# Performance work log

Hardware: AMD Instinct MI355X
Metric: run time of the kernel (lower is better)

Reference implementation:

```python
import jax, jax.numpy as jnp
import numpy as np

N, K, H = 20000, 32, 128
DIN = 3 * H   # num_hidden + num_in = 128 + 256
FF = 4 * H
SCALE = 30.0
EPS = 1e-5


def setup_inputs() -> dict:
    key = jax.random.key(0)
    ks = jax.random.split(key, 32)
    s = 0.05
    w = lambda k, shp: jax.random.normal(k, shp, dtype=jnp.float32) * s
    return {
        "h_V": jax.random.normal(ks[0], (N, H), dtype=jnp.float32),
        "h_E": jax.random.normal(ks[1], (N, K, H), dtype=jnp.float32),
        "mask_V": jnp.ones((N,), dtype=jnp.float32),
        "mask_attend": jnp.ones((N, K), dtype=jnp.float32),
        # message MLP 1 (weights stored [in, out])
        "W1_w": w(ks[2], (DIN, H)), "W1_b": jnp.zeros((H,)),
        "W2_w": w(ks[3], (H, H)),   "W2_b": jnp.zeros((H,)),
        "W3_w": w(ks[4], (H, H)),   "W3_b": jnp.zeros((H,)),
        # message MLP 2
        "W11_w": w(ks[5], (DIN, H)), "W11_b": jnp.zeros((H,)),
        "W12_w": w(ks[6], (H, H)),   "W12_b": jnp.zeros((H,)),
        "W13_w": w(ks[7], (H, H)),   "W13_b": jnp.zeros((H,)),
        # position-wise FFN
        "Win_w": w(ks[8], (H, FF)),  "Win_b": jnp.zeros((FF,)),
        "Wout_w": w(ks[9], (FF, H)), "Wout_b": jnp.zeros((H,)),
        # LayerNorms
        "ln1_g": jnp.ones((H,)), "ln1_b": jnp.zeros((H,)),
        "ln2_g": jnp.ones((H,)), "ln2_b": jnp.zeros((H,)),
        "ln3_g": jnp.ones((H,)), "ln3_b": jnp.zeros((H,)),
        "E_idx": jax.random.randint(ks[10], (N, K), 0, N),
    }


def _ln(x, g, b):
    m = jnp.mean(x, -1, keepdims=True)
    v = jnp.mean(jnp.square(x - m), -1, keepdims=True)
    return (x - m) * jax.lax.rsqrt(v + EPS) * g + b


def _gelu(x):
    return jax.nn.gelu(x, approximate=False)  # torch default (erf) GELU


def reference(h_V, h_E, mask_V, mask_attend,
              W1_w, W1_b, W2_w, W2_b, W3_w, W3_b,
              W11_w, W11_b, W12_w, W12_b, W13_w, W13_b,
              Win_w, Win_b, Wout_w, Wout_b,
              ln1_g, ln1_b, ln2_g, ln2_b, ln3_g, ln3_b,
              E_idx):
    n, k = E_idx.shape

    def edge_feats(hv):
        nbr = hv[E_idx]  # [N,K,H] gather of neighbor node features
        hv_exp = jnp.broadcast_to(hv[:, None, :], (n, k, hv.shape[-1]))
        return jnp.concatenate([hv_exp, h_E, nbr], -1)  # [N,K,3H]

    # --- node update ---
    h_EV = edge_feats(h_V)
    msg = _gelu(h_EV @ W1_w + W1_b)
    msg = _gelu(msg @ W2_w + W2_b)
    msg = msg @ W3_w + W3_b
    msg = mask_attend[..., None] * msg
    dh = jnp.sum(msg, axis=-2) / SCALE
    hV = _ln(h_V + dh, ln1_g, ln1_b)
    dh = _gelu(hV @ Win_w + Win_b) @ Wout_w + Wout_b
    hV = _ln(hV + dh, ln2_g, ln2_b)
    hV = mask_V[:, None] * hV

    # --- edge update ---
    h_EV = edge_feats(hV)
    msg = _gelu(h_EV @ W11_w + W11_b)
    msg = _gelu(msg @ W12_w + W12_b)
    msg = msg @ W13_w + W13_b
    hE = _ln(h_E + msg, ln3_g, ln3_b)
    return (hV, hE)
```

## Files before the change

### kernel.cpp

```cpp
#include <hip/hip_runtime.h>
#include <hip/hip_bf16.h>
#include <cstdint>
#include <cstddef>

#define NN 20000
#define KK 32
#define HH 128
#define FFD 512
#define LN_EPS 1e-5f

typedef __attribute__((ext_vector_type(8))) short bf16x8;
typedef __attribute__((ext_vector_type(4))) float f32x4;

__device__ __forceinline__ short f2b(float f){
  __hip_bfloat16 h = __float2bfloat16(f);
  return __builtin_bit_cast(short, h);
}
__device__ __forceinline__ float b2f(short s){
  union { unsigned int u; float f; } v; v.u = ((unsigned int)(unsigned short)s) << 16; return v.f;
}
__device__ __forceinline__ unsigned int pk2(float a, float b){
  return (unsigned int)(unsigned short)f2b(a) | ((unsigned int)(unsigned short)f2b(b) << 16);
}
__device__ __forceinline__ float gelu_fast(float x){
  float u = x * __builtin_fmaf(0.10294278f, x*x, 2.3022082f);
  float e = __builtin_amdgcn_exp2f(u);
  float r = __builtin_amdgcn_rcpf(1.0f + e);
  return __builtin_fmaf(-x, r, x);
}
__device__ __forceinline__ f32x4 MFMA(bf16x8 a, bf16x8 b, f32x4 c){
  return __builtin_amdgcn_mfma_f32_16x16x32_bf16(a, b, c, 0, 0, 0);
}

__global__ __launch_bounds__(256) void enc_pack(
    const float* __restrict__ W1, const float* __restrict__ W2, const float* __restrict__ W3,
    const float* __restrict__ W11, const float* __restrict__ W12, const float* __restrict__ W13,
    const float* __restrict__ Win, const float* __restrict__ Wout,
    short* __restrict__ pk)
{
  const int stride = gridDim.x * blockDim.x;
  for (int idx = blockIdx.x*blockDim.x + threadIdx.x; idx < 294912; idx += stride){
    const float* src = W2; int srow = 0, k, n, NT, NCOLS, base;
    if (idx < 163840){
      int slot = idx >> 14, e = idx & 16383;
      k = e >> 7; n = e & 127; NT = 8; NCOLS = 128; base = slot << 14;
      switch (slot){
        case 0: src = W1;  srow = 0;   break;
        case 1: src = W1;  srow = 256; break;
        case 2: src = W1;  srow = 128; break;
        case 3: src = W2;  srow = 0;   break;
        case 4: src = W3;  srow = 0;   break;
        case 5: src = W11; srow = 0;   break;
        case 6: src = W11; srow = 256; break;
        case 7: src = W11; srow = 128; break;
        case 8: src = W12; srow = 0;   break;
        default: src = W13; srow = 0;  break;
      }
    } else if (idx < 229376){
      int e = idx - 163840; k = e >> 9; n = e & 511; NT = 32; NCOLS = 512; src = Win; base = 163840;
    } else {
      int e = idx - 229376; k = e >> 7; n = e & 127; NT = 8; NCOLS = 128; src = Wout; base = 229376;
    }
    float v = src[(srow + k)*NCOLS + n];
    int out = base + (((k>>5)*NT + (n>>4))*64 + ((k>>3)&3)*16 + (n&15))*8 + (k&7);
    pk[out] = f2b(v);
  }
}

__global__ __launch_bounds__(256, 2) void enc_proj(
    const float* __restrict__ X, const short* __restrict__ pkU, const short* __restrict__ pkZ,
    const float* __restrict__ biasU, short* __restrict__ U, short* __restrict__ Z)
{
  const int lane = threadIdx.x & 63, w = threadIdx.x >> 6;
  const int kgrp = lane >> 4, ccol = lane & 15;
  const int row0 = blockIdx.x*64 + w*16;
  const int arow = row0 + (lane & 15);
  f32x4 accU[8], accZ[8];
  #pragma unroll
  for (int nf=0;nf<8;nf++){ accU[nf] = (f32x4){0,0,0,0}; accZ[nf] = (f32x4){0,0,0,0}; }
  #pragma unroll
  for (int kt=0;kt<4;kt++){
    bf16x8 af = {0,0,0,0,0,0,0,0};
    if (arow < NN){
      const float4* p = (const float4*)(X + (size_t)arow*HH + kt*32 + kgrp*8);
      float4 v0 = p[0], v1 = p[1];
      af[0]=f2b(v0.x); af[1]=f2b(v0.y); af[2]=f2b(v0.z); af[3]=f2b(v0.w);
      af[4]=f2b(v1.x); af[5]=f2b(v1.y); af[6]=f2b(v1.z); af[7]=f2b(v1.w);
    }
    #pragma unroll
    for (int nf=0;nf<8;nf++){
      bf16x8 bu = *(const bf16x8*)(pkU + (((kt<<3)+nf)*64 + lane)*8);
      accU[nf] = MFMA(af, bu, accU[nf]);
      bf16x8 bz = *(const bf16x8*)(pkZ + (((kt<<3)+nf)*64 + lane)*8);
      accZ[nf] = MFMA(af, bz, accZ[nf]);
    }
  }
  #pragma unroll
  for (int nf=0;nf<8;nf++){
    #pragma unroll
    for (int r=0;r<4;r++){
      int grow = row0 + kgrp*4 + r;
      if (grow < NN){
        int col = nf*16 + ccol;
        U[(size_t)grow*HH + col] = f2b(accU[nf][r] + biasU[col]);
        Z[(size_t)grow*HH + col] = f2b(accZ[nf][r]);
      }
    }
  }
}

#define LSTR 136
template<int PASS>
__global__ __launch_bounds__(256, 3) void enc_mlp3(
    const float* __restrict__ hE,
    const short* __restrict__ Ub, const short* __restrict__ Zb,
    const int*  __restrict__ Eidx,
    const float* __restrict__ maskAtt,
    const float* __restrict__ hV,
    const float* __restrict__ lnG, const float* __restrict__ lnB,
    const short* __restrict__ pkL1,
    const short* __restrict__ pkL2, const float* __restrict__ bias2,
    const short* __restrict__ pkL3, const float* __restrict__ bias3,
    float* __restrict__ outP)
{
  __shared__ __align__(16) short sBuf[64*LSTR];
  __shared__ __align__(16) short sW[16384];
  __shared__ float sB23[256];
  __shared__ float sPart[4][128];

  const int i0 = blockIdx.x*2;
  const int t = threadIdx.x;
  const int lane = t & 63, w = t >> 6;
  const int kgrp = lane >> 4, ccol = lane & 15;
  const int g = w >> 1;
  const int rw = w*16;

  const int zrow = rw + (lane >> 2);
  const int seg0 = lane & 3;
  const int j = Eidx[i0*KK + zrow];
  const int4* zsrc = (const int4*)(Zb + (size_t)j*HH);

  float ureg[8];
  #pragma unroll
  for (int nf=0; nf<8; nf++) ureg[nf] = b2f(Ub[(size_t)(i0+g)*HH + nf*16 + ccol]);

  float mreg[4] = {0,0,0,0};
  if (PASS == 0){
    const float4 mv = *(const float4*)(maskAtt + i0*KK + rw + kgrp*4);
    mreg[0]=mv.x; mreg[1]=mv.y; mreg[2]=mv.z; mreg[3]=mv.w;
  }

  sB23[t] = (t < 128) ? bias2[t] : bias3[t-128];

  #pragma unroll
  for (int it=0; it<8; it++){
    int idx = it*256 + t;
    *(int4*)(sW + idx*8) = *(const int4*)(pkL1 + idx*8);
  }

  {
    const float4* src = (const float4*)(hE + ((size_t)i0*KK + rw)*HH);
    #pragma unroll
    for (int it=0; it<8; it++){
      int r = it*2 + (lane>>5);
      int c4 = lane & 31;
      float4 v = src[r*32 + c4];
      uint2 p; p.x = pk2(v.x, v.y); p.y = pk2(v.z, v.w);
      *(uint2*)(sBuf + (rw + r)*LSTR + c4*4) = p;
    }
  }
  __syncthreads();

  const short* sRow = sBuf + (rw + ccol)*LSTR;
  f32x4 acc[8];

  #pragma unroll
  for (int nf=0;nf<8;nf++) acc[nf] = (f32x4){ureg[nf],ureg[nf],ureg[nf],ureg[nf]};
  #pragma unroll
  for (int kt=0;kt<4;kt++){
    bf16x8 af = *(const bf16x8*)(sRow + kt*32 + kgrp*8);
    #pragma unroll
    for (int nf=0;nf<8;nf++){
      bf16x8 b = *(const bf16x8*)(sW + (((kt<<3)+nf)*64 + lane)*8);
      acc[nf] = MFMA(af, b, acc[nf]);
    }
  }
  {
    int4 z0 = zsrc[seg0];
    int4 z1 = zsrc[seg0 + 4];
    int4 z2 = zsrc[seg0 + 8];
    int4 z3 = zsrc[seg0 + 12];
    *(int4*)(sBuf + zrow*LSTR + (seg0     )*8) = z0;
    *(int4*)(sBuf + zrow*LSTR + (seg0 + 4 )*8) = z1;
    *(int4*)(sBuf + zrow*LSTR + (seg0 + 8 )*8) = z2;
    *(int4*)(sBuf + zrow*LSTR + (seg0 + 12)*8) = z3;
  }
  __syncthreads();
  #pragma unroll
  for (int it=0; it<8; it++){
    int idx = it*256 + t;
    *(int4*)(sW + idx*8) = *(const int4*)(pkL2 + idx*8);
  }
  #pragma unroll
  for (int nf=0;nf<8;nf++){
    #pragma unroll
    for (int r=0;r<4;r++){
      short* p = sBuf + (rw + kgrp*4 + r)*LSTR + nf*16 + ccol;
      float v = acc[nf][r] + b2f(*p);
      *p = f2b(gelu_fast(v));
    }
  }
  __syncthreads();

  #pragma unroll
  for (int nf=0;nf<8;nf++){
    float b2v = sB23[nf*16 + ccol];
    acc[nf] = (f32x4){b2v,b2v,b2v,b2v};
  }
  #pragma unroll
  for (int kt=0;kt<4;kt++){
    bf16x8 af = *(const bf16x8*)(sRow + kt*32 + kgrp*8);
    #pragma unroll
    for (int nf=0;nf<8;nf++){
      bf16x8 b = *(const bf16x8*)(sW + (((kt<<3)+nf)*64 + lane)*8);
      acc[nf] = MFMA(af, b, acc[nf]);
    }
  }
  __syncthreads();
  #pragma unroll
  for (int it=0; it<8; it++){
    int idx = it*256 + t;
    *(int4*)(sW + idx*8) = *(const int4*)(pkL3 + idx*8);
  }
  #pragma unroll
  for (int nf=0;nf<8;nf++){
    #pragma unroll
    for (int r=0;r<4;r++){
      short* p = sBuf + (rw + kgrp*4 + r)*LSTR + nf*16 + ccol;
      *p = f2b(gelu_fast(acc[nf][r]));
    }
  }
  __syncthreads();

  #pragma unroll
  for (int nf=0;nf<8;nf++){
    float b3v = sB23[128 + nf*16 + ccol];
    acc[nf] = (f32x4){b3v,b3v,b3v,b3v};
  }
  #pragma unroll
  for (int kt=0;kt<4;kt++){
    bf16x8 af = *(const bf16x8*)(sRow + kt*32 + kgrp*8);
    #pragma unroll
    for (int nf=0;nf<8;nf++){
      bf16x8 b = *(const bf16x8*)(sW + (((kt<<3)+nf)*64 + lane)*8);
      acc[nf] = MFMA(af, b, acc[nf]);
    }
  }

  if (PASS == 0){
    float ps[8];
    #pragma unroll
    for (int nf=0;nf<8;nf++){
      float s = 0.f;
      #pragma unroll
      for (int r=0;r<4;r++) s = __builtin_fmaf(acc[nf][r], mreg[r], s);
      s += __shfl_xor(s, 16);
      s += __shfl_xor(s, 32);
      ps[nf] = s;
    }
    if (kgrp == 0){
      #pragma unroll
      for (int nf=0;nf<8;nf++) sPart[w][nf*16 + ccol] = ps[nf];
    }
    __syncthreads();
    if ((w & 1) == 0){
      const int node = i0 + (w>>1);
      float c0 = sPart[w][lane]    + sPart[w+1][lane];
      float c1 = sPart[w][64+lane] + sPart[w+1][64+lane];
      float x0 = hV[(size_t)node*HH + lane]      + c0*(1.0f/30.0f);
      float x1 = hV[(size_t)node*HH + 64 + lane] + c1*(1.0f/30.0f);
      float sm = x0 + x1, sq = x0*x0 + x1*x1;
      #pragma unroll
      for (int off=1; off<64; off<<=1){
        sm += __shfl_xor(sm, off);
        sq += __shfl_xor(sq, off);
      }
      float mean = sm*(1.f/128.f);
      float var  = sq*(1.f/128.f) - mean*mean;
      float inv  = rsqrtf(var + LN_EPS);
      outP[(size_t)node*HH + lane]      = (x0-mean)*inv*lnG[lane]    + lnB[lane];
      outP[(size_t)node*HH + 64 + lane] = (x1-mean)*inv*lnG[64+lane] + lnB[64+lane];
    }
  } else {
    float rs[4] = {0,0,0,0}, rq[4] = {0,0,0,0};
    #pragma unroll
    for (int nf=0;nf<8;nf++){
      #pragma unroll
      for (int r=0;r<4;r++){
        int row = rw + kgrp*4 + r, col = nf*16 + ccol;
        float x = acc[nf][r] + hE[((size_t)(i0*KK + row))*HH + col];
        acc[nf][r] = x;
        rs[r] += x; rq[r] += x*x;
      }
    }
    #pragma unroll
    for (int off=1; off<16; off<<=1){
      #pragma unroll
      for (int r=0;r<4;r++){
        rs[r] += __shfl_xor(rs[r], off);
        rq[r] += __shfl_xor(rq[r], off);
      }
    }
    #pragma unroll
    for (int r=0;r<4;r++){
      float mean = rs[r]*(1.f/128.f);
      float var  = rq[r]*(1.f/128.f) - mean*mean;
      float inv  = rsqrtf(var + LN_EPS);
      #pragma unroll
      for (int nf=0;nf<8;nf++){
        int row = rw + kgrp*4 + r, col = nf*16 + ccol;
        outP[((size_t)(i0*KK + row))*HH + col] = (acc[nf][r]-mean)*inv*lnG[col] + lnB[col];
      }
    }
  }
}

__global__ __launch_bounds__(256, 2) void enc_ffn(
    const float* __restrict__ X,
    const short* __restrict__ pkWin, const float* __restrict__ bin,
    const short* __restrict__ pkWout, const float* __restrict__ bout,
    const float* __restrict__ g2, const float* __restrict__ b2ln,
    const float* __restrict__ maskV,
    float* __restrict__ out)
{
  __shared__ short sT[64*512];
  const int t = threadIdx.x, lane = t & 63, w = t >> 6;
  const int kgrp = lane >> 4, ccol = lane & 15;
  const int row0 = blockIdx.x*64;
  const int arow = row0 + w*16 + (lane & 15);
  f32x4 acc[32];
  #pragma unroll
  for (int nf=0;nf<32;nf++) acc[nf] = (f32x4){0,0,0,0};
  #pragma unroll
  for (int kt=0;kt<4;kt++){
    bf16x8 af = {0,0,0,0,0,0,0,0};
    if (arow < NN){
      const float4* p = (const float4*)(X + (size_t)arow*HH + kt*32 + kgrp*8);
      float4 v0 = p[0], v1 = p[1];
      af[0]=f2b(v0.x); af[1]=f2b(v0.y); af[2]=f2b(v0.z); af[3]=f2b(v0.w);
      af[4]=f2b(v1.x); af[5]=f2b(v1.y); af[6]=f2b(v1.z); af[7]=f2b(v1.w);
    }
    #pragma unroll
    for (int nf=0;nf<32;nf++){
      bf16x8 b = *(const bf16x8*)(pkWin + ((size_t)((kt<<5)+nf)*64 + lane)*8);
      acc[nf] = MFMA(af, b, acc[nf]);
    }
  }
  #pragma unroll
  for (int nf=0;nf<32;nf++){
    #pragma unroll
    for (int r=0;r<4;r++){
      int rl = w*16 + kgrp*4 + r, col = nf*16 + ccol;
      sT[rl*512 + (col ^ ((rl&7)<<3))] = f2b(gelu_fast(acc[nf][r] + bin[col]));
    }
  }
  f32x4 a2[8];
  #pragma unroll
  for (int nf=0;nf<8;nf++) a2[nf] = (f32x4){0,0,0,0};
  const int rl_a = w*16 + (lane & 15);
  #pragma unroll
  for (int kt=0;kt<16;kt++){
    int base = kt*32 + kgrp*8;
    bf16x8 af = *(const bf16x8*)(sT + rl_a*512 + (base ^ ((rl_a&7)<<3)));
    #pragma unroll
    for (int nf=0;nf<8;nf++){
      bf16x8 b = *(const bf16x8*)(pkWout + (((kt<<3)+nf)*64 + lane)*8);
      a2[nf] = MFMA(af, b, a2[nf]);
    }
  }
  float rsum[4] = {0,0,0,0}, rsq[4] = {0,0,0,0};
  #pragma unroll
  for (int nf=0;nf<8;nf++){
    #pragma unroll
    for (int r=0;r<4;r++){
      int grow = row0 + w*16 + kgrp*4 + r, col = nf*16 + ccol;
      float prev = (grow < NN) ? X[(size_t)grow*HH + col] : 0.f;
      float x = a2[nf][r] + bout[col] + prev;
      a2[nf][r] = x;
      rsum[r] += x; rsq[r] += x*x;
    }
  }
  #pragma unroll
  for (int off=1; off<16; off<<=1){
    #pragma unroll
    for (int r=0;r<4;r++){
      rsum[r] += __shfl_xor(rsum[r], off);
      rsq[r]  += __shfl_xor(rsq[r], off);
    }
  }
  #pragma unroll
  for (int r=0;r<4;r++){
    int grow = row0 + w*16 + kgrp*4 + r;
    float mean = rsum[r]*(1.f/128.f);
    float var  = rsq[r]*(1.f/128.f) - mean*mean;
    float inv  = rsqrtf(var + LN_EPS);
    float mv   = (grow < NN) ? maskV[grow] : 0.f;
    #pragma unroll
    for (int nf=0;nf<8;nf++){
      int col = nf*16 + ccol;
      if (grow < NN)
        out[(size_t)grow*HH + col] = mv * ((a2[nf][r]-mean)*inv*g2[col] + b2ln[col]);
    }
  }
}

extern "C" void kernel_launch(void* const* d_in, const int* in_sizes, int n_in,
                              void* d_out, int out_size, void* d_ws, size_t ws_size,
                              hipStream_t stream)
{
  const float* h_V   = (const float*)d_in[0];
  const float* h_E   = (const float*)d_in[1];
  const float* maskV = (const float*)d_in[2];
  const float* maskA = (const float*)d_in[3];
  const float* W1w  = (const float*)d_in[4];  const float* W1b  = (const float*)d_in[5];
  const float* W2w  = (const float*)d_in[6];  const float* W2b  = (const float*)d_in[7];
  const float* W3w  = (const float*)d_in[8];  const float* W3b  = (const float*)d_in[9];
  const float* W11w = (const float*)d_in[10]; const float* W11b = (const float*)d_in[11];
  const float* W12w = (const float*)d_in[12]; const float* W12b = (const float*)d_in[13];
  const float* W13w = (const float*)d_in[14]; const float* W13b = (const float*)d_in[15];
  const float* Winw = (const float*)d_in[16]; const float* Winb = (const float*)d_in[17];
  const float* Woutw= (const float*)d_in[18]; const float* Woutb= (const float*)d_in[19];
  const float* ln1g = (const float*)d_in[20]; const float* ln1b = (const float*)d_in[21];
  const float* ln2g = (const float*)d_in[22]; const float* ln2b = (const float*)d_in[23];
  const float* ln3g = (const float*)d_in[24]; const float* ln3b = (const float*)d_in[25];
  const int*   Eidx = (const int*)d_in[26];

  float* outV = (float*)d_out;
  float* outE = outV + (size_t)NN*HH;

  char* ws = (char*)d_ws;
  short* pk = (short*)ws;
  const short* pkW1a  = pk + 0*16384;
  const short* pkW1c  = pk + 1*16384;
  const short* pkW1bb = pk + 2*16384;
  const short* pkW2   = pk + 3*16384;
  const short* pkW3   = pk + 4*16384;
  const short* pkW11a = pk + 5*16384;
  const short* pkW11c = pk + 6*16384;
  const short* pkW11bb= pk + 7*16384;
  const short* pkW12  = pk + 8*16384;
  const short* pkW13  = pk + 9*16384;
  const short* pkWin  = pk + 163840;
  const short* pkWout = pk + 229376;

  short* U1 = (short*)(ws + 1048576);
  short* Z1 = (short*)(ws + 6291456);
  short* U2 = (short*)(ws + 11534336);
  short* Z2 = (short*)(ws + 16777216);
  float* hVmid = (float*)(ws + 22020096);

  enc_pack<<<288, 256, 0, stream>>>(W1w, W2w, W3w, W11w, W12w, W13w, Winw, Woutw, pk);
  enc_proj<<<313, 256, 0, stream>>>(h_V, pkW1a, pkW1c, W1b, U1, Z1);
  enc_mlp3<0><<<NN/2, 256, 0, stream>>>(h_E, U1, Z1, Eidx, maskA, h_V,
                                        ln1g, ln1b, pkW1bb, pkW2, W2b, pkW3, W3b, hVmid);
  enc_ffn<<<313, 256, 0, stream>>>(hVmid, pkWin, Winb, pkWout, Woutb,
                                   ln2g, ln2b, maskV, outV);
  enc_proj<<<313, 256, 0, stream>>>(outV, pkW11a, pkW11c, W11b, U2, Z2);
  enc_mlp3<1><<<NN/2, 256, 0, stream>>>(h_E, U2, Z2, Eidx, nullptr, nullptr,
                                        ln3g, ln3b, pkW11bb, pkW12, W12b, pkW13, W13b, outE);
}
```

Baseline: 439.3 us.

## Process four nodes per 512-thread block in edge MLP kernel

Doubles the block size of the fused edge MLP kernel so each block handles four nodes (128 edge rows) instead of two. Each staged weight matrix in shared memory is then reused across twice as many rows, halving weight-staging traffic per edge. Bias and U-term additions move from accumulator initialisation into the epilogues, and the Z/U/mask loads are deferred, to reduce live registers. Shared memory per block grows and the launch bound changes to 512 threads with 4 blocks requested, which may be infeasible and could hurt occupancy or cause spills.

Result: faster. 424.6 us (-3.3%).

```diff
diff --git a/kernel.cpp b/kernel.cpp
--- a/kernel.cpp
+++ b/kernel.cpp
@@ -111,7 +111,7 @@
 
 #define LSTR 136
 template<int PASS>
-__global__ __launch_bounds__(256, 3) void enc_mlp3(
+__global__ __launch_bounds__(512, 4) void enc_mlp3(
     const float* __restrict__ hE,
     const short* __restrict__ Ub, const short* __restrict__ Zb,
     const int*  __restrict__ Eidx,
@@ -123,38 +123,23 @@
     const short* __restrict__ pkL3, const float* __restrict__ bias3,
     float* __restrict__ outP)
 {
-  __shared__ __align__(16) short sBuf[64*LSTR];
+  __shared__ __align__(16) short sBuf[128*LSTR];
   __shared__ __align__(16) short sW[16384];
   __shared__ float sB23[256];
-  __shared__ float sPart[4][128];
-
-  const int i0 = blockIdx.x*2;
+  __shared__ float sPart[8][128];
+
+  const int i0 = blockIdx.x*4;
   const int t = threadIdx.x;
   const int lane = t & 63, w = t >> 6;
   const int kgrp = lane >> 4, ccol = lane & 15;
-  const int g = w >> 1;
+  const int node = i0 + (w >> 1);
   const int rw = w*16;
 
-  const int zrow = rw + (lane >> 2);
-  const int seg0 = lane & 3;
-  const int j = Eidx[i0*KK + zrow];
-  const int4* zsrc = (const int4*)(Zb + (size_t)j*HH);
-
-  float ureg[8];
-  #pragma unroll
-  for (int nf=0; nf<8; nf++) ureg[nf] = b2f(Ub[(size_t)(i0+g)*HH + nf*16 + ccol]);
-
-  float mreg[4] = {0,0,0,0};
-  if (PASS == 0){
-    const float4 mv = *(const float4*)(maskAtt + i0*KK + rw + kgrp*4);
-    mreg[0]=mv.x; mreg[1]=mv.y; mreg[2]=mv.z; mreg[3]=mv.w;
-  }
-
-  sB23[t] = (t < 128) ? bias2[t] : bias3[t-128];
-
-  #pragma unroll
-  for (int it=0; it<8; it++){
-    int idx = it*256 + t;
+  if (t < 256) sB23[t] = (t < 128) ? bias2[t] : bias3[t-128];
+
+  #pragma unroll
+  for (int it=0; it<4; it++){
+    int idx = it*512 + t;
     *(int4*)(sW + idx*8) = *(const int4*)(pkL1 + idx*8);
   }
 
@@ -175,7 +160,7 @@
   f32x4 acc[8];
 
   #pragma unroll
-  for (int nf=0;nf<8;nf++) acc[nf] = (f32x4){ureg[nf],ureg[nf],ureg[nf],ureg[nf]};
+  for (int nf=0;nf<8;nf++) acc[nf] = (f32x4){0,0,0,0};
   #pragma unroll
   for (int kt=0;kt<4;kt++){
     bf16x8 af = *(const bf16x8*)(sRow + kt*32 + kgrp*8);
@@ -186,6 +171,10 @@
     }
   }
   {
+    const int zrow = rw + (lane >> 2);
+    const int seg0 = lane & 3;
+    const int jj = Eidx[i0*KK + zrow];
+    const int4* zsrc = (const int4*)(Zb + (size_t)jj*HH);
     int4 z0 = zsrc[seg0];
     int4 z1 = zsrc[seg0 + 4];
     int4 z2 = zsrc[seg0 + 8];
@@ -197,26 +186,52 @@
   }
   __syncthreads();
   #pragma unroll
-  for (int it=0; it<8; it++){
-    int idx = it*256 + t;
+  for (int it=0; it<4; it++){
+    int idx = it*512 + t;
     *(int4*)(sW + idx*8) = *(const int4*)(pkL2 + idx*8);
   }
   #pragma unroll
   for (int nf=0;nf<8;nf++){
+    float uv = b2f(Ub[(size_t)node*HH + nf*16 + ccol]);
     #pragma unroll
     for (int r=0;r<4;r++){
       short* p = sBuf + (rw + kgrp*4 + r)*LSTR + nf*16 + ccol;
-      float v = acc[nf][r] + b2f(*p);
+      float v = acc[nf][r] + uv + b2f(*p);
       *p = f2b(gelu_fast(v));
     }
   }
   __syncthreads();
 
+  #pragma unroll
+  for (int nf=0;nf<8;nf++) acc[nf] = (f32x4){0,0,0,0};
+  #pragma unroll
+  for (int kt=0;kt<4;kt++){
+    bf16x8 af = *(const bf16x8*)(sRow + kt*32 + kgrp*8);
+    #pragma unroll
+    for (int nf=0;nf<8;nf++){
+      bf16x8 b = *(const bf16x8*)(sW + (((kt<<3)+nf)*64 + lane)*8);
+      acc[nf] = MFMA(af, b, acc[nf]);
+    }
+  }
+  __syncthreads();
+  #pragma unroll
+  for (int it=0; it<4; it++){
+    int idx = it*512 + t;
+    *(int4*)(sW + idx*8) = *(const int4*)(pkL3 + idx*8);
+  }
   #pragma unroll
   for (int nf=0;nf<8;nf++){
     float b2v = sB23[nf*16 + ccol];
-    acc[nf] = (f32x4){b2v,b2v,b2v,b2v};
-  }
+    #pragma unroll
+    for (int r=0;r<4;r++){
+      short* p = sBuf + (rw + kgrp*4 + r)*LSTR + nf*16 + ccol;
+      *p = f2b(gelu_fast(acc[nf][r] + b2v));
+    }
+  }
+  __syncthreads();
+
+  #pragma unroll
+  for (int nf=0;nf<8;nf++) acc[nf] = (f32x4){0,0,0,0};
   #pragma unroll
   for (int kt=0;kt<4;kt++){
     bf16x8 af = *(const bf16x8*)(sRow + kt*32 + kgrp*8);
@@ -226,55 +241,25 @@
       acc[nf] = MFMA(af, b, acc[nf]);
     }
   }
-  __syncthreads();
-  #pragma unroll
-  for (int it=0; it<8; it++){
-    int idx = it*256 + t;
-    *(int4*)(sW + idx*8) = *(const int4*)(pkL3 + idx*8);
-  }
-  #pragma unroll
-  for (int nf=0;nf<8;nf++){
-    #pragma unroll
-    for (int r=0;r<4;r++){
-      short* p = sBuf + (rw + kgrp*4 + r)*LSTR + nf*16 + ccol;
-      *p = f2b(gelu_fast(acc[nf][r]));
-    }
-  }
-  __syncthreads();
-
-  #pragma unroll
-  for (int nf=0;nf<8;nf++){
-    float b3v = sB23[128 + nf*16 + ccol];
-    acc[nf] = (f32x4){b3v,b3v,b3v,b3v};
-  }
-  #pragma unroll
-  for (int kt=0;kt<4;kt++){
-    bf16x8 af = *(const bf16x8*)(sRow + kt*32 + kgrp*8);
-    #pragma unroll
-    for (int nf=0;nf<8;nf++){
-      bf16x8 b = *(const bf16x8*)(sW + (((kt<<3)+nf)*64 + lane)*8);
-      acc[nf] = MFMA(af, b, acc[nf]);
-    }
-  }
 
   if (PASS == 0){
-    float ps[8];
-    #pragma unroll
-    for (int nf=0;nf<8;nf++){
+    float m[4];
+    {
+      const float4 mv = *(const float4*)(maskAtt + i0*KK + rw + kgrp*4);
+      m[0]=mv.x; m[1]=mv.y; m[2]=mv.z; m[3]=mv.w;
+    }
+    #pragma unroll
+    for (int nf=0;nf<8;nf++){
+      float b3v = sB23[128 + nf*16 + ccol];
       float s = 0.f;
       #pragma unroll
-      for (int r=0;r<4;r++) s = __builtin_fmaf(acc[nf][r], mreg[r], s);
+      for (int r=0;r<4;r++) s = __builtin_fmaf(acc[nf][r] + b3v, m[r], s);
       s += __shfl_xor(s, 16);
       s += __shfl_xor(s, 32);
-      ps[nf] = s;
-    }
-    if (kgrp == 0){
-      #pragma unroll
-      for (int nf=0;nf<8;nf++) sPart[w][nf*16 + ccol] = ps[nf];
+      if (kgrp == 0) sPart[w][nf*16 + ccol] = s;
     }
     __syncthreads();
     if ((w & 1) == 0){
-      const int node = i0 + (w>>1);
       float c0 = sPart[w][lane]    + sPart[w+1][lane];
       float c1 = sPart[w][64+lane] + sPart[w+1][64+lane];
       float x0 = hV[(size_t)node*HH + lane]      + c0*(1.0f/30.0f);
@@ -295,10 +280,11 @@
     float rs[4] = {0,0,0,0}, rq[4] = {0,0,0,0};
     #pragma unroll
     for (int nf=0;nf<8;nf++){
+      float b3v = sB23[128 + nf*16 + ccol];
       #pragma unroll
       for (int r=0;r<4;r++){
         int row = rw + kgrp*4 + r, col = nf*16 + ccol;
-        float x = acc[nf][r] + hE[((size_t)(i0*KK + row))*HH + col];
+        float x = acc[nf][r] + b3v + hE[((size_t)(i0*KK + row))*HH + col];
         acc[nf][r] = x;
         rs[r] += x; rq[r] += x*x;
       }
@@ -461,11 +447,11 @@
 
   enc_pack<<<288, 256, 0, stream>>>(W1w, W2w, W3w, W11w, W12w, W13w, Winw, Woutw, pk);
   enc_proj<<<313, 256, 0, stream>>>(h_V, pkW1a, pkW1c, W1b, U1, Z1);
-  enc_mlp3<0><<<NN/2, 256, 0, stream>>>(h_E, U1, Z1, Eidx, maskA, h_V,
+  enc_mlp3<0><<<NN/4, 512, 0, stream>>>(h_E, U1, Z1, Eidx, maskA, h_V,
                                         ln1g, ln1b, pkW1bb, pkW2, W2b, pkW3, W3b, hVmid);
   enc_ffn<<<313, 256, 0, stream>>>(hVmid, pkWin, Winb, pkWout, Woutb,
                                    ln2g, ln2b, maskV, outV);
   enc_proj<<<313, 256, 0, stream>>>(outV, pkW11a, pkW11c, W11b, U2, Z2);
-  enc_mlp3<1><<<NN/2, 256, 0, stream>>>(h_E, U2, Z2, Eidx, nullptr, nullptr,
+  enc_mlp3<1><<<NN/4, 512, 0, stream>>>(h_E, U2, Z2, Eidx, nullptr, nullptr,
                                         ln3g, ln3b, pkW11bb, pkW12, W12b, pkW13, W13b, outE);
 }
```
